# Kernel optimization log

Measured on AMD Instinct MI355X. Metric: run time of the kernel, lower is better.

Reference implementation:

```python
import jax, jax.numpy as jnp
import numpy as np

EPS = 1e-12
NUM_HEADS = 16
FEATURE_DIM = 16
HEAD_DIM = 64


def setup_inputs() -> dict:
    key = jax.random.key(0)
    k1, k2, k3, k4, k5 = jax.random.split(key, 5)
    b, l, d_model = 2, 2048, 1024
    scale = 0.02
    return {
        "hidden_states": jax.random.normal(k1, (b, l, d_model), jnp.float32),
        "Wq": jax.random.normal(k2, (FEATURE_DIM * NUM_HEADS, d_model), jnp.float32) * scale,
        "Wk": jax.random.normal(k3, (FEATURE_DIM * NUM_HEADS, d_model), jnp.float32) * scale,
        "Wv": jax.random.normal(k4, (NUM_HEADS * HEAD_DIM, d_model), jnp.float32) * scale,
        "Wo": jax.random.normal(k5, (d_model, NUM_HEADS * HEAD_DIM), jnp.float32) * scale,
    }


def reference(hidden_states, Wq, Wk, Wv, Wo):
    b, l, d_model = hidden_states.shape
    h, fd, hd = NUM_HEADS, FEATURE_DIM, HEAD_DIM
    # projections (no bias), split heads: (b, h, l, dim)
    q = (hidden_states @ Wq.T).reshape(b, l, h, fd).transpose(0, 2, 1, 3)
    k = (hidden_states @ Wk.T).reshape(b, l, h, fd).transpose(0, 2, 1, 3)
    v = (hidden_states @ Wv.T).reshape(b, l, h, hd).transpose(0, 2, 1, 3)
    # feature map is identity (default FeatureMap)
    # quadratic causal linear attention
    A_qk = jnp.einsum("bhnd,bhmd->bhnm", q, k)  # [b,h,l,l]
    A_qk = jnp.tril(A_qk)
    y = jnp.einsum("bhnm,bhme->bhne", A_qk, v)  # [b,h,l,hd]
    # denominator: q . cumsum(k)
    z = 1.0 / (jnp.einsum("bhld,bhld->bhl", q, jnp.cumsum(k, axis=2)) + EPS)
    y = y * z[..., None]
    # merge heads and output projection
    y = y.transpose(0, 2, 1, 3).reshape(b, l, h * hd)
    return y @ Wo.T
```

## Files before the change

kernel.cpp:

```cpp
#include <hip/hip_runtime.h>
#include <hip/hip_bf16.h>

#define NH 16
#define FD 16
#define HD 64
#define BATCH 2
#define SEQ 2048
#define DM 1024
#define ROWS (BATCH * SEQ)
#define CHUNK 128
#define NCH (SEQ / CHUNK)
#define NBH (BATCH * NH)

typedef __hip_bfloat16 bf16;
typedef __attribute__((ext_vector_type(8))) short short8;
typedef __attribute__((ext_vector_type(4))) float f32x4;

__device__ inline float bfbits(unsigned int h) {
  union { unsigned int u; float f; } c; c.u = h << 16; return c.f;
}
__device__ inline unsigned short f2bf(float x) {
  bf16 h = __float2bfloat16(x);
  return *(unsigned short*)&h;
}

__device__ inline void load8(const void* src, size_t idx, int isf32, float* out) {
  if (isf32) {
    const float* p = (const float*)src + idx;
    float4 a = *(const float4*)p;
    float4 b = *(const float4*)(p + 4);
    out[0] = a.x; out[1] = a.y; out[2] = a.z; out[3] = a.w;
    out[4] = b.x; out[5] = b.y; out[6] = b.z; out[7] = b.w;
  } else {
    const uint4 w = *(const uint4*)((const unsigned short*)src + idx);
    out[0] = bfbits(w.x & 0xffffu); out[1] = bfbits(w.x >> 16);
    out[2] = bfbits(w.y & 0xffffu); out[3] = bfbits(w.y >> 16);
    out[4] = bfbits(w.z & 0xffffu); out[5] = bfbits(w.z >> 16);
    out[6] = bfbits(w.w & 0xffffu); out[7] = bfbits(w.w >> 16);
  }
}

__device__ inline void gload16(const void* g, void* l) {
  __builtin_amdgcn_global_load_lds(
      (const __attribute__((address_space(1))) unsigned int*)g,
      (__attribute__((address_space(3))) unsigned int*)l, 16, 0, 0);
}

__global__ __launch_bounds__(256) void detect_dtype(const unsigned int* __restrict__ w,
                                                    int* __restrict__ flag) {
  __shared__ int red[256];
  int cnt = 0;
  for (int i = threadIdx.x; i < 4096; i += 256) {
    unsigned int e = (w[i] >> 7) & 0xFFu;
    cnt += (e >= 0x90u) ? 1 : 0;
  }
  red[threadIdx.x] = cnt;
  __syncthreads();
  for (int s = 128; s > 0; s >>= 1) {
    if (threadIdx.x < s) red[threadIdx.x] += red[threadIdx.x + s];
    __syncthreads();
  }
  if (threadIdx.x == 0) *flag = (red[0] > 64) ? 1 : 0;
}

__global__ __launch_bounds__(256, 2) void gemm_qk5(const void* __restrict__ A,
                                                   const void* __restrict__ Wq,
                                                   const void* __restrict__ Wk,
                                                   const int* __restrict__ flagp,
                                                   float* __restrict__ qf,
                                                   float* __restrict__ kf) {
  const int isf32 = *flagp;
  __shared__ float smem[9216];
  const int tid = threadIdx.x;
  const int h = tid >> 7;
  const int ltid = tid & 127;
  float* As = smem + h * 2304;
  float* Bs = smem + 4608 + h * 2304;
  const int m0 = blockIdx.x * 64;
  const int isK = blockIdx.y >> 2;
  const int n0 = (blockIdx.y & 3) * 64;
  const void* B = isK ? Wk : Wq;
  float* C = isK ? kf : qf;
  const int tx = ltid & 7;
  const int ty = ltid >> 3;
  const int lm = ltid >> 1, lcH = (ltid & 1) * 16;
  const int kbase = h * 512;
  double dacc[8][4];
#pragma unroll
  for (int i = 0; i < 8; ++i)
#pragma unroll
    for (int n = 0; n < 4; ++n) dacc[i][n] = 0.0;

  float av[16], bv[16];
  load8(A, (size_t)(m0 + lm) * DM + kbase + lcH, isf32, &av[0]);
  load8(A, (size_t)(m0 + lm) * DM + kbase + lcH + 8, isf32, &av[8]);
  load8(B, (size_t)(n0 + lm) * DM + kbase + lcH, isf32, &bv[0]);
  load8(B, (size_t)(n0 + lm) * DM + kbase + lcH + 8, isf32, &bv[8]);

  for (int t = 0; t < 16; ++t) {
    __syncthreads();
    *(float4*)&As[lm * 36 + lcH] = *(float4*)&av[0];
    *(float4*)&As[lm * 36 + lcH + 4] = *(float4*)&av[4];
    *(float4*)&As[lm * 36 + lcH + 8] = *(float4*)&av[8];
    *(float4*)&As[lm * 36 + lcH + 12] = *(float4*)&av[12];
    *(float4*)&Bs[lm * 36 + lcH] = *(float4*)&bv[0];
    *(float4*)&Bs[lm * 36 + lcH + 4] = *(float4*)&bv[4];
    *(float4*)&Bs[lm * 36 + lcH + 8] = *(float4*)&bv[8];
    *(float4*)&Bs[lm * 36 + lcH + 12] = *(float4*)&bv[12];
    __syncthreads();
    if (t < 15) {
      int kt = kbase + (t + 1) * 32;
      load8(A, (size_t)(m0 + lm) * DM + kt + lcH, isf32, &av[0]);
      load8(A, (size_t)(m0 + lm) * DM + kt + lcH + 8, isf32, &av[8]);
      load8(B, (size_t)(n0 + lm) * DM + kt + lcH, isf32, &bv[0]);
      load8(B, (size_t)(n0 + lm) * DM + kt + lcH + 8, isf32, &bv[8]);
    }
    for (int kk = 0; kk < 32; kk += 4) {
      float4 ar[8], br[4];
#pragma unroll
      for (int i = 0; i < 8; ++i) ar[i] = *(const float4*)&As[(tx + 8 * i) * 36 + kk];
#pragma unroll
      for (int n = 0; n < 4; ++n) br[n] = *(const float4*)&Bs[(ty * 4 + n) * 36 + kk];
      float facc[8][4] = {};
#pragma unroll
      for (int j = 0; j < 4; ++j) {
#pragma unroll
        for (int i = 0; i < 8; ++i) {
          float a = ((const float*)&ar[i])[j];
#pragma unroll
          for (int n = 0; n < 4; ++n)
            facc[i][n] += a * ((const float*)&br[n])[j];
        }
      }
#pragma unroll
      for (int i = 0; i < 8; ++i)
#pragma unroll
        for (int n = 0; n < 4; ++n) dacc[i][n] += (double)facc[i][n];
    }
  }

  double* dbl = (double*)smem;
  __syncthreads();
  if (h == 1) {
#pragma unroll
    for (int i = 0; i < 8; ++i)
#pragma unroll
      for (int n = 0; n < 4; ++n) dbl[ltid * 32 + i * 4 + n] = dacc[i][n];
  }
  __syncthreads();
  if (h == 0) {
#pragma unroll
    for (int i = 0; i < 8; ++i) {
#pragma unroll
      for (int n = 0; n < 4; ++n) dacc[i][n] += dbl[ltid * 32 + i * 4 + n];
      int row = m0 + tx + 8 * i;
      float4 o;
      o.x = (float)dacc[i][0]; o.y = (float)dacc[i][1];
      o.z = (float)dacc[i][2]; o.w = (float)dacc[i][3];
      *(float4*)&C[(size_t)row * 256 + n0 + ty * 4] = o;
    }
  }
}

template <int MODE>
__global__ __launch_bounds__(256) void gemm_mfma(const void* __restrict__ Ap,
                                                 const void* __restrict__ Bp,
                                                 const int* __restrict__ flagp,
                                                 void* __restrict__ Cp) {
  const int isf32 = *flagp;
  const int aF32 = (MODE == 0) ? isf32 : 0;
  const int bF32 = isf32;
  __shared__ unsigned short As[128 * 32];
  __shared__ unsigned short Bs[64 * 32];
  const int tid = threadIdx.x;
  const int wave = tid >> 6, lane = tid & 63;
  const int m0 = blockIdx.x * 128, n0 = blockIdx.y * 64;
  const int lrow = lane >> 2, lch = (lane & 3) * 8;
  const int wm = wave >> 1, wn = wave & 1;
  const int mlane = lane & 15, kgrp = lane >> 4;
  const unsigned short* Ab = (const unsigned short*)Ap;
  const unsigned short* Bb = (const unsigned short*)Bp;
  f32x4 acc[4][2];
#pragma unroll
  for (int t = 0; t < 4; ++t)
#pragma unroll
    for (int u = 0; u < 2; ++u) acc[t][u] = (f32x4){0.f, 0.f, 0.f, 0.f};

  for (int k0 = 0; k0 < DM; k0 += 32) {
    __syncthreads();
    if (!aF32) {
      const int r0 = wave * 32;
#pragma unroll
      for (int j = 0; j < 2; ++j) {
        const void* g = Ab + (size_t)(m0 + r0 + j * 16 + lrow) * DM + k0 + lch;
        gload16(g, &As[(r0 + j * 16) * 32]);
      }
    } else {
      for (int c = tid; c < 512; c += 256) {
        int r = c >> 2, cc = (c & 3) * 8;
        float v8[8];
        load8(Ap, (size_t)(m0 + r) * DM + k0 + cc, 1, v8);
        unsigned int w[4];
#pragma unroll
        for (int g2 = 0; g2 < 4; ++g2)
          w[g2] = (unsigned)f2bf(v8[2 * g2]) | ((unsigned)f2bf(v8[2 * g2 + 1]) << 16);
        *(uint4*)&As[r * 32 + cc] = *(uint4*)w;
      }
    }
    if (!bF32) {
      const void* g = Bb + (size_t)(n0 + wave * 16 + lrow) * DM + k0 + lch;
      gload16(g, &Bs[(wave * 16) * 32]);
    } else {
      {
        int c = tid;
        int r = c >> 2, cc = (c & 3) * 8;
        float v8[8];
        load8(Bp, (size_t)(n0 + r) * DM + k0 + cc, 1, v8);
        unsigned int w[4];
#pragma unroll
        for (int g2 = 0; g2 < 4; ++g2)
          w[g2] = (unsigned)f2bf(v8[2 * g2]) | ((unsigned)f2bf(v8[2 * g2 + 1]) << 16);
        *(uint4*)&Bs[r * 32 + cc] = *(uint4*)w;
      }
    }
    __syncthreads();

    short8 af[4], bfr[2];
#pragma unroll
    for (int t = 0; t < 4; ++t)
      af[t] = *(const short8*)&As[(wm * 64 + t * 16 + mlane) * 32 + kgrp * 8];
#pragma unroll
    for (int u = 0; u < 2; ++u)
      bfr[u] = *(const short8*)&Bs[(wn * 32 + u * 16 + mlane) * 32 + kgrp * 8];
#pragma unroll
    for (int t = 0; t < 4; ++t)
#pragma unroll
      for (int u = 0; u < 2; ++u)
        acc[t][u] = __builtin_amdgcn_mfma_f32_16x16x32_bf16(af[t], bfr[u], acc[t][u], 0, 0, 0);
  }

#pragma unroll
  for (int t = 0; t < 4; ++t)
#pragma unroll
    for (int u = 0; u < 2; ++u)
#pragma unroll
      for (int r = 0; r < 4; ++r) {
        int row = m0 + wm * 64 + t * 16 + kgrp * 4 + r;
        int col = n0 + wn * 32 + u * 16 + mlane;
        float v = acc[t][u][r];
        if (MODE == 0) {
          ((unsigned short*)Cp)[(size_t)row * DM + col] = f2bf(v);
        } else if (isf32) {
          ((float*)Cp)[(size_t)row * DM + col] = v;
        } else {
          ((unsigned short*)Cp)[(size_t)row * DM + col] = f2bf(v);
        }
      }
}

__global__ __launch_bounds__(256) void attn_intra(const float* __restrict__ qf,
                                                  const float* __restrict__ kf,
                                                  const unsigned short* __restrict__ vfb,
                                                  unsigned short* __restrict__ yib,
                                                  float* __restrict__ Sc,
                                                  double* __restrict__ Kc) {
  __shared__ float qc[CHUNK][20];
  __shared__ float kc[CHUNK][20];
  __shared__ float vc[CHUNK][68];
  const int bh = blockIdx.x >> 4;
  const int c = blockIdx.x & 15;
  const int b = bh >> 4, h = bh & 15;
  const int bl = c * CHUNK;
  const int tid = threadIdx.x;

  for (int idx = tid; idx < CHUNK * FD / 4; idx += 256) {
    int r = idx >> 2, f4 = (idx & 3) * 4;
    size_t g = ((size_t)(b * SEQ + bl + r)) * (NH * FD) + h * FD + f4;
    *(float4*)&qc[r][f4] = *(const float4*)&qf[g];
    *(float4*)&kc[r][f4] = *(const float4*)&kf[g];
  }
  for (int idx = tid; idx < CHUNK * HD / 8; idx += 256) {
    int r = idx >> 3, e8 = (idx & 7) * 8;
    uint4 w = *(const uint4*)&vfb[((size_t)(b * SEQ + bl + r)) * (NH * HD) + h * HD + e8];
    vc[r][e8 + 0] = bfbits(w.x & 0xffffu); vc[r][e8 + 1] = bfbits(w.x >> 16);
    vc[r][e8 + 2] = bfbits(w.y & 0xffffu); vc[r][e8 + 3] = bfbits(w.y >> 16);
    vc[r][e8 + 4] = bfbits(w.z & 0xffffu); vc[r][e8 + 5] = bfbits(w.z >> 16);
    vc[r][e8 + 6] = bfbits(w.w & 0xffffu); vc[r][e8 + 7] = bfbits(w.w >> 16);
  }
  __syncthreads();

  const int p = tid >> 2;
  const int n0 = 2 * p, n1 = 2 * p + 1;
  const int e0 = (tid & 3) * 16;
  float q0r[16], q1r[16];
#pragma unroll
  for (int d = 0; d < 16; ++d) { q0r[d] = qc[n0][d]; q1r[d] = qc[n1][d]; }
  float y0[16], y1[16];
#pragma unroll
  for (int e = 0; e < 16; ++e) { y0[e] = 0.f; y1[e] = 0.f; }

  for (int m = 0; m <= n1; ++m) {
    float kd[16], vv[16];
#pragma unroll
    for (int d = 0; d < 16; ++d) kd[d] = kc[m][d];
#pragma unroll
    for (int e = 0; e < 16; ++e) vv[e] = vc[m][e0 + e];
    float d0 = 0.f, d1 = 0.f;
#pragma unroll
    for (int d = 0; d < 16; ++d) { d0 += q0r[d] * kd[d]; d1 += q1r[d] * kd[d]; }
    if (m > n0) d0 = 0.f;
#pragma unroll
    for (int e = 0; e < 16; ++e) { y0[e] += d0 * vv[e]; y1[e] += d1 * vv[e]; }
  }
  const size_t ybase = (size_t)bh * SEQ + bl;
  {
    unsigned int w[4];
#pragma unroll
    for (int g = 0; g < 4; ++g)
      w[g] = (unsigned)f2bf(y0[2 * g]) | ((unsigned)f2bf(y0[2 * g + 1]) << 16);
    *(uint4*)&yib[(ybase + n0) * HD + e0] = *(uint4*)w;
#pragma unroll
    for (int g = 0; g < 4; ++g)
      w[g] = (unsigned)f2bf(y0[8 + 2 * g]) | ((unsigned)f2bf(y0[9 + 2 * g]) << 16);
    *(uint4*)&yib[(ybase + n0) * HD + e0 + 8] = *(uint4*)w;
#pragma unroll
    for (int g = 0; g < 4; ++g)
      w[g] = (unsigned)f2bf(y1[2 * g]) | ((unsigned)f2bf(y1[2 * g + 1]) << 16);
    *(uint4*)&yib[(ybase + n1) * HD + e0] = *(uint4*)w;
#pragma unroll
    for (int g = 0; g < 4; ++g)
      w[g] = (unsigned)f2bf(y1[8 + 2 * g]) | ((unsigned)f2bf(y1[9 + 2 * g]) << 16);
    *(uint4*)&yib[(ybase + n1) * HD + e0 + 8] = *(uint4*)w;
  }

  float* Scp = Sc + ((size_t)bh * NCH + c) * (FD * HD);
  for (int idx = tid; idx < FD * HD; idx += 256) {
    int d = idx >> 6, e = idx & 63;
    float s = 0.f;
    for (int m = 0; m < CHUNK; ++m) s += kc[m][d] * vc[m][e];
    Scp[idx] = s;
  }
  if (tid < FD) {
    double ks = 0.0;
    for (int m = 0; m < CHUNK; ++m) ks += (double)kc[m][tid];
    Kc[((size_t)bh * NCH + c) * FD + tid] = ks;
  }
}

__global__ __launch_bounds__(256) void scan_states(float* __restrict__ Sc,
                                                   double* __restrict__ Kc) {
  const int bh = blockIdx.x;
  const int tid = threadIdx.x;
  float4 acc = make_float4(0.f, 0.f, 0.f, 0.f);
  size_t base = (size_t)bh * NCH * (FD * HD) + (size_t)tid * 4;
  for (int c = 0; c < NCH; ++c) {
    float4* p = (float4*)(Sc + base + (size_t)c * (FD * HD));
    float4 v = *p;
    *p = acc;
    acc.x += v.x; acc.y += v.y; acc.z += v.z; acc.w += v.w;
  }
  if (tid < FD) {
    double a = 0.0;
    for (int c = 0; c < NCH; ++c) {
      size_t i = ((size_t)bh * NCH + c) * FD + tid;
      double t = Kc[i];
      Kc[i] = a;
      a += t;
    }
  }
}

__global__ __launch_bounds__(256) void attn_finish(const float* __restrict__ qf,
                                                   const float* __restrict__ kf,
                                                   const unsigned short* __restrict__ yib,
                                                   const float* __restrict__ Sc,
                                                   const double* __restrict__ Kc,
                                                   unsigned short* __restrict__ yob) {
  __shared__ float qc[CHUNK][20];
  __shared__ float kc[CHUNK][20];
  __shared__ float Sp[FD][HD];
  __shared__ double cs[CHUNK][17];
  __shared__ double zl[CHUNK];
  __shared__ double ksp[FD];
  const int bh = blockIdx.x >> 4;
  const int c = blockIdx.x & 15;
  const int b = bh >> 4, h = bh & 15;
  const int bl = c * CHUNK;
  const int tid = threadIdx.x;

  for (int idx = tid; idx < CHUNK * FD / 4; idx += 256) {
    int r = idx >> 2, f4 = (idx & 3) * 4;
    size_t g = ((size_t)(b * SEQ + bl + r)) * (NH * FD) + h * FD + f4;
    *(float4*)&qc[r][f4] = *(const float4*)&qf[g];
    *(float4*)&kc[r][f4] = *(const float4*)&kf[g];
  }
  const float* Scp = Sc + ((size_t)bh * NCH + c) * (FD * HD);
  for (int idx = tid; idx < FD * HD / 4; idx += 256) {
    int d = idx >> 4, e4 = (idx & 15) * 4;
    *(float4*)&Sp[d][e4] = *(const float4*)&Scp[(size_t)d * HD + e4];
  }
  if (tid < FD) ksp[tid] = Kc[((size_t)bh * NCH + c) * FD + tid];
  __syncthreads();

  if (tid < FD) {
    double run = ksp[tid];
    for (int m = 0; m < CHUNK; ++m) {
      run += (double)kc[m][tid];
      cs[m][tid] = run;
    }
  }
  __syncthreads();
  if (tid < CHUNK) {
    double dn = 0.0;
#pragma unroll
    for (int d = 0; d < 16; ++d) dn += (double)qc[tid][d] * cs[tid][d];
    zl[tid] = 1.0 / (dn + 1e-12);
  }
  __syncthreads();

  for (int idx = tid; idx < CHUNK * HD / 8; idx += 256) {
    int n = idx >> 3, e8 = (idx & 7) * 8;
    uint4 w = *(const uint4*)&yib[((size_t)bh * SEQ + bl + n) * HD + e8];
    float yv[8] = {bfbits(w.x & 0xffffu), bfbits(w.x >> 16),
                   bfbits(w.y & 0xffffu), bfbits(w.y >> 16),
                   bfbits(w.z & 0xffffu), bfbits(w.z >> 16),
                   bfbits(w.w & 0xffffu), bfbits(w.w >> 16)};
    double z = zl[n];
    unsigned int o[4];
#pragma unroll
    for (int jp = 0; jp < 4; ++jp) {
      int e = e8 + 2 * jp;
      float i0 = 0.f, i1 = 0.f;
#pragma unroll
      for (int d = 0; d < 16; ++d) {
        i0 += qc[n][d] * Sp[d][e];
        i1 += qc[n][d] * Sp[d][e + 1];
      }
      float r0 = (float)(((double)(yv[2 * jp] + i0)) * z);
      float r1 = (float)(((double)(yv[2 * jp + 1] + i1)) * z);
      o[jp] = (unsigned)f2bf(r0) | ((unsigned)f2bf(r1) << 16);
    }
    *(uint4*)&yob[((size_t)(b * SEQ + bl + n)) * (NH * HD) + h * HD + e8] = *(uint4*)o;
  }
}

extern "C" void kernel_launch(void* const* d_in, const int* in_sizes, int n_in,
                              void* d_out, int out_size, void* d_ws, size_t ws_size,
                              hipStream_t stream) {
  (void)in_sizes; (void)n_in; (void)out_size; (void)ws_size;
  const void* hs = d_in[0];
  const void* Wq = d_in[1];
  const void* Wk = d_in[2];
  const void* Wv = d_in[3];
  const void* Wo = d_in[4];

  char* ws = (char*)d_ws;
  float* qf = (float*)(ws);
  float* kf = (float*)(ws + (4u << 20));
  unsigned short* vfb = (unsigned short*)(ws + (8u << 20));
  unsigned short* yob = vfb;
  unsigned short* yib = (unsigned short*)(ws + (16u << 20));
  float* Sc = (float*)(ws + (24u << 20));
  double* Kc = (double*)(ws + (26u << 20));
  int* flag = (int*)(ws + (26u << 20) + 65536);

  detect_dtype<<<1, 256, 0, stream>>>((const unsigned int*)hs, flag);
  gemm_qk5<<<dim3(ROWS / 64, 8), 256, 0, stream>>>(hs, Wq, Wk, flag, qf, kf);
  gemm_mfma<0><<<dim3(ROWS / 128, 1024 / 64), 256, 0, stream>>>(hs, Wv, flag, vfb);
  attn_intra<<<NBH * NCH, 256, 0, stream>>>(qf, kf, vfb, yib, Sc, Kc);
  scan_states<<<NBH, 256, 0, stream>>>(Sc, Kc);
  attn_finish<<<NBH * NCH, 256, 0, stream>>>(qf, kf, yib, Sc, Kc, yob);
  gemm_mfma<1><<<dim3(ROWS / 128, 1024 / 64), 256, 0, stream>>>(yob, Wo, flag, d_out);
}
```

Baseline: 298.6 us.

## Merge Q/K and V projections into one interleaved launch, read B from global

Combines the fp64-accumulated Q/K projection kernel and the MFMA V projection kernel into a single launch whose even blocks do Q/K tiles and odd blocks do V tiles. This removes one launch and lets the two workloads share the GPU concurrently. The Q/K path no longer stages weights in shared memory; each thread loads its B slices directly from global memory. That shrinks LDS use so more blocks can be resident (launch bound raised to 4), but it adds redundant global/cache traffic. The double reduction buffer is also transposed to avoid bank conflicts, and the output GEMM is specialized to bf16 activations.

```diff
diff --git a/kernel.cpp b/kernel.cpp
--- a/kernel.cpp
+++ b/kernel.cpp
@@ -40,6 +40,15 @@
   }
 }
 
+__device__ inline float4 load4(const void* src, size_t idx, int isf32) {
+  if (isf32) return *((const float4*)((const float*)src + idx));
+  uint2 w = *(const uint2*)((const unsigned short*)src + idx);
+  float4 r;
+  r.x = bfbits(w.x & 0xffffu); r.y = bfbits(w.x >> 16);
+  r.z = bfbits(w.y & 0xffffu); r.w = bfbits(w.y >> 16);
+  return r;
+}
+
 __device__ inline void gload16(const void* g, void* l) {
   __builtin_amdgcn_global_load_lds(
       (const __attribute__((address_space(1))) unsigned int*)g,
@@ -63,113 +72,188 @@
   if (threadIdx.x == 0) *flag = (red[0] > 64) ? 1 : 0;
 }
 
-__global__ __launch_bounds__(256, 2) void gemm_qk5(const void* __restrict__ A,
-                                                   const void* __restrict__ Wq,
-                                                   const void* __restrict__ Wk,
-                                                   const int* __restrict__ flagp,
-                                                   float* __restrict__ qf,
-                                                   float* __restrict__ kf) {
+__global__ __launch_bounds__(256, 4) void stage1(const void* __restrict__ hs,
+                                                 const void* __restrict__ Wq,
+                                                 const void* __restrict__ Wk,
+                                                 const void* __restrict__ Wv,
+                                                 const int* __restrict__ flagp,
+                                                 float* __restrict__ qf,
+                                                 float* __restrict__ kf,
+                                                 unsigned short* __restrict__ vfb) {
+  __shared__ double2 smem_d2[2048];
   const int isf32 = *flagp;
-  __shared__ float smem[9216];
   const int tid = threadIdx.x;
-  const int h = tid >> 7;
-  const int ltid = tid & 127;
-  float* As = smem + h * 2304;
-  float* Bs = smem + 4608 + h * 2304;
-  const int m0 = blockIdx.x * 64;
-  const int isK = blockIdx.y >> 2;
-  const int n0 = (blockIdx.y & 3) * 64;
-  const void* B = isK ? Wk : Wq;
-  float* C = isK ? kf : qf;
-  const int tx = ltid & 7;
-  const int ty = ltid >> 3;
-  const int lm = ltid >> 1, lcH = (ltid & 1) * 16;
-  const int kbase = h * 512;
-  double dacc[8][4];
-#pragma unroll
-  for (int i = 0; i < 8; ++i)
-#pragma unroll
-    for (int n = 0; n < 4; ++n) dacc[i][n] = 0.0;
-
-  float av[16], bv[16];
-  load8(A, (size_t)(m0 + lm) * DM + kbase + lcH, isf32, &av[0]);
-  load8(A, (size_t)(m0 + lm) * DM + kbase + lcH + 8, isf32, &av[8]);
-  load8(B, (size_t)(n0 + lm) * DM + kbase + lcH, isf32, &bv[0]);
-  load8(B, (size_t)(n0 + lm) * DM + kbase + lcH + 8, isf32, &bv[8]);
-
-  for (int t = 0; t < 16; ++t) {
+
+  if ((blockIdx.x & 1) == 0) {
+    const int qid = blockIdx.x >> 1;
+    const int m0 = (qid & 63) * 64;
+    const int y = qid >> 6;
+    const int isK = y >> 2;
+    const int n0 = (y & 3) * 64;
+    const void* A = hs;
+    const void* B = isK ? Wk : Wq;
+    float* C = isK ? kf : qf;
+    const int h = tid >> 7;
+    const int ltid = tid & 127;
+    float* As = (float*)smem_d2 + h * 2304;
+    const int tx = ltid & 7;
+    const int ty = ltid >> 3;
+    const int lm = ltid >> 1, lcH = (ltid & 1) * 16;
+    const int kbase = h * 512;
+    double dacc[8][4];
+#pragma unroll
+    for (int i = 0; i < 8; ++i)
+#pragma unroll
+      for (int n = 0; n < 4; ++n) dacc[i][n] = 0.0;
+
+    float av[16];
+    load8(A, (size_t)(m0 + lm) * DM + kbase + lcH, isf32, &av[0]);
+    load8(A, (size_t)(m0 + lm) * DM + kbase + lcH + 8, isf32, &av[8]);
+
+    for (int t = 0; t < 16; ++t) {
+      __syncthreads();
+      *(float4*)&As[lm * 36 + lcH] = *(float4*)&av[0];
+      *(float4*)&As[lm * 36 + lcH + 4] = *(float4*)&av[4];
+      *(float4*)&As[lm * 36 + lcH + 8] = *(float4*)&av[8];
+      *(float4*)&As[lm * 36 + lcH + 12] = *(float4*)&av[12];
+      __syncthreads();
+      if (t < 15) {
+        int kt = kbase + (t + 1) * 32;
+        load8(A, (size_t)(m0 + lm) * DM + kt + lcH, isf32, &av[0]);
+        load8(A, (size_t)(m0 + lm) * DM + kt + lcH + 8, isf32, &av[8]);
+      }
+      const size_t bkt = kbase + t * 32;
+      for (int kk = 0; kk < 32; kk += 4) {
+        float4 ar[8], br[4];
+#pragma unroll
+        for (int i = 0; i < 8; ++i) ar[i] = *(const float4*)&As[(tx + 8 * i) * 36 + kk];
+#pragma unroll
+        for (int n = 0; n < 4; ++n)
+          br[n] = load4(B, (size_t)(n0 + ty * 4 + n) * DM + bkt + kk, isf32);
+        float facc[8][4] = {};
+#pragma unroll
+        for (int j = 0; j < 4; ++j) {
+#pragma unroll
+          for (int i = 0; i < 8; ++i) {
+            float a = ((const float*)&ar[i])[j];
+#pragma unroll
+            for (int n = 0; n < 4; ++n)
+              facc[i][n] += a * ((const float*)&br[n])[j];
+          }
+        }
+#pragma unroll
+        for (int i = 0; i < 8; ++i)
+#pragma unroll
+          for (int n = 0; n < 4; ++n) dacc[i][n] += (double)facc[i][n];
+      }
+    }
+
+    double* dbl = (double*)smem_d2;
     __syncthreads();
-    *(float4*)&As[lm * 36 + lcH] = *(float4*)&av[0];
-    *(float4*)&As[lm * 36 + lcH + 4] = *(float4*)&av[4];
-    *(float4*)&As[lm * 36 + lcH + 8] = *(float4*)&av[8];
-    *(float4*)&As[lm * 36 + lcH + 12] = *(float4*)&av[12];
-    *(float4*)&Bs[lm * 36 + lcH] = *(float4*)&bv[0];
-    *(float4*)&Bs[lm * 36 + lcH + 4] = *(float4*)&bv[4];
-    *(float4*)&Bs[lm * 36 + lcH + 8] = *(float4*)&bv[8];
-    *(float4*)&Bs[lm * 36 + lcH + 12] = *(float4*)&bv[12];
+    if (h == 1) {
+#pragma unroll
+      for (int i = 0; i < 8; ++i)
+#pragma unroll
+        for (int n = 0; n < 4; ++n) dbl[(i * 4 + n) * 128 + ltid] = dacc[i][n];
+    }
     __syncthreads();
-    if (t < 15) {
-      int kt = kbase + (t + 1) * 32;
-      load8(A, (size_t)(m0 + lm) * DM + kt + lcH, isf32, &av[0]);
-      load8(A, (size_t)(m0 + lm) * DM + kt + lcH + 8, isf32, &av[8]);
-      load8(B, (size_t)(n0 + lm) * DM + kt + lcH, isf32, &bv[0]);
-      load8(B, (size_t)(n0 + lm) * DM + kt + lcH + 8, isf32, &bv[8]);
-    }
-    for (int kk = 0; kk < 32; kk += 4) {
-      float4 ar[8], br[4];
-#pragma unroll
-      for (int i = 0; i < 8; ++i) ar[i] = *(const float4*)&As[(tx + 8 * i) * 36 + kk];
-#pragma unroll
-      for (int n = 0; n < 4; ++n) br[n] = *(const float4*)&Bs[(ty * 4 + n) * 36 + kk];
-      float facc[8][4] = {};
-#pragma unroll
-      for (int j = 0; j < 4; ++j) {
-#pragma unroll
-        for (int i = 0; i < 8; ++i) {
-          float a = ((const float*)&ar[i])[j];
-#pragma unroll
-          for (int n = 0; n < 4; ++n)
-            facc[i][n] += a * ((const float*)&br[n])[j];
+    if (h == 0) {
+#pragma unroll
+      for (int i = 0; i < 8; ++i) {
+#pragma unroll
+        for (int n = 0; n < 4; ++n) dacc[i][n] += dbl[(i * 4 + n) * 128 + ltid];
+        int row = m0 + tx + 8 * i;
+        float4 o;
+        o.x = (float)dacc[i][0]; o.y = (float)dacc[i][1];
+        o.z = (float)dacc[i][2]; o.w = (float)dacc[i][3];
+        *(float4*)&C[(size_t)row * 256 + n0 + ty * 4] = o;
+      }
+    }
+  } else {
+    const int vid = blockIdx.x >> 1;
+    const int m0 = (vid & 31) * 128;
+    const int n0 = (vid >> 5) * 64;
+    unsigned short* As = (unsigned short*)smem_d2;
+    unsigned short* Bs = As + 128 * 32;
+    const int wave = tid >> 6, lane = tid & 63;
+    const int lrow = lane >> 2, lch = (lane & 3) * 8;
+    const int wm = wave >> 1, wn = wave & 1;
+    const int mlane = lane & 15, kgrp = lane >> 4;
+    const unsigned short* Ab = (const unsigned short*)hs;
+    const unsigned short* Bb = (const unsigned short*)Wv;
+    f32x4 acc[4][2];
+#pragma unroll
+    for (int t = 0; t < 4; ++t)
+#pragma unroll
+      for (int u = 0; u < 2; ++u) acc[t][u] = (f32x4){0.f, 0.f, 0.f, 0.f};
+
+    for (int k0 = 0; k0 < DM; k0 += 32) {
+      __syncthreads();
+      if (!isf32) {
+        const int r0 = wave * 32;
+#pragma unroll
+        for (int j = 0; j < 2; ++j) {
+          const void* g = Ab + (size_t)(m0 + r0 + j * 16 + lrow) * DM + k0 + lch;
+          gload16(g, &As[(r0 + j * 16) * 32]);
         }
-      }
-#pragma unroll
-      for (int i = 0; i < 8; ++i)
-#pragma unroll
-        for (int n = 0; n < 4; ++n) dacc[i][n] += (double)facc[i][n];
-    }
-  }
-
-  double* dbl = (double*)smem;
-  __syncthreads();
-  if (h == 1) {
-#pragma unroll
-    for (int i = 0; i < 8; ++i)
-#pragma unroll
-      for (int n = 0; n < 4; ++n) dbl[ltid * 32 + i * 4 + n] = dacc[i][n];
-  }
-  __syncthreads();
-  if (h == 0) {
-#pragma unroll
-    for (int i = 0; i < 8; ++i) {
-#pragma unroll
-      for (int n = 0; n < 4; ++n) dacc[i][n] += dbl[ltid * 32 + i * 4 + n];
-      int row = m0 + tx + 8 * i;
-      float4 o;
-      o.x = (float)dacc[i][0]; o.y = (float)dacc[i][1];
-      o.z = (float)dacc[i][2]; o.w = (float)dacc[i][3];
-      *(float4*)&C[(size_t)row * 256 + n0 + ty * 4] = o;
-    }
-  }
-}
-
-template <int MODE>
-__global__ __launch_bounds__(256) void gemm_mfma(const void* __restrict__ Ap,
-                                                 const void* __restrict__ Bp,
-                                                 const int* __restrict__ flagp,
-                                                 void* __restrict__ Cp) {
+        const void* g = Bb + (size_t)(n0 + wave * 16 + lrow) * DM + k0 + lch;
+        gload16(g, &Bs[(wave * 16) * 32]);
+      } else {
+        for (int c = tid; c < 512; c += 256) {
+          int r = c >> 2, cc = (c & 3) * 8;
+          float v8[8];
+          load8(hs, (size_t)(m0 + r) * DM + k0 + cc, 1, v8);
+          unsigned int w[4];
+#pragma unroll
+          for (int g2 = 0; g2 < 4; ++g2)
+            w[g2] = (unsigned)f2bf(v8[2 * g2]) | ((unsigned)f2bf(v8[2 * g2 + 1]) << 16);
+          *(uint4*)&As[r * 32 + cc] = *(uint4*)w;
+        }
+        {
+          int r = tid >> 2, cc = (tid & 3) * 8;
+          float v8[8];
+          load8(Wv, (size_t)(n0 + r) * DM + k0 + cc, 1, v8);
+          unsigned int w[4];
+#pragma unroll
+          for (int g2 = 0; g2 < 4; ++g2)
+            w[g2] = (unsigned)f2bf(v8[2 * g2]) | ((unsigned)f2bf(v8[2 * g2 + 1]) << 16);
+          *(uint4*)&Bs[r * 32 + cc] = *(uint4*)w;
+        }
+      }
+      __syncthreads();
+
+      short8 af[4], bfr[2];
+#pragma unroll
+      for (int t = 0; t < 4; ++t)
+        af[t] = *(const short8*)&As[(wm * 64 + t * 16 + mlane) * 32 + kgrp * 8];
+#pragma unroll
+      for (int u = 0; u < 2; ++u)
+        bfr[u] = *(const short8*)&Bs[(wn * 32 + u * 16 + mlane) * 32 + kgrp * 8];
+#pragma unroll
+      for (int t = 0; t < 4; ++t)
+#pragma unroll
+        for (int u = 0; u < 2; ++u)
+          acc[t][u] = __builtin_amdgcn_mfma_f32_16x16x32_bf16(af[t], bfr[u], acc[t][u], 0, 0, 0);
+    }
+
+#pragma unroll
+    for (int t = 0; t < 4; ++t)
+#pragma unroll
+      for (int u = 0; u < 2; ++u)
+#pragma unroll
+        for (int r = 0; r < 4; ++r) {
+          int row = m0 + wm * 64 + t * 16 + kgrp * 4 + r;
+          int col = n0 + wn * 32 + u * 16 + mlane;
+          vfb[(size_t)row * DM + col] = f2bf(acc[t][u][r]);
+        }
+  }
+}
+
+__global__ __launch_bounds__(256) void gemm_o(const unsigned short* __restrict__ Ap,
+                                              const void* __restrict__ Bp,
+                                              const int* __restrict__ flagp,
+                                              void* __restrict__ Cp) {
   const int isf32 = *flagp;
-  const int aF32 = (MODE == 0) ? isf32 : 0;
-  const int bF32 = isf32;
   __shared__ unsigned short As[128 * 32];
   __shared__ unsigned short Bs[64 * 32];
   const int tid = threadIdx.x;
@@ -178,7 +262,6 @@
   const int lrow = lane >> 2, lch = (lane & 3) * 8;
   const int wm = wave >> 1, wn = wave & 1;
   const int mlane = lane & 15, kgrp = lane >> 4;
-  const unsigned short* Ab = (const unsigned short*)Ap;
   const unsigned short* Bb = (const unsigned short*)Bp;
   f32x4 acc[4][2];
 #pragma unroll
@@ -188,40 +271,26 @@
 
   for (int k0 = 0; k0 < DM; k0 += 32) {
     __syncthreads();
-    if (!aF32) {
+    {
       const int r0 = wave * 32;
 #pragma unroll
       for (int j = 0; j < 2; ++j) {
-        const void* g = Ab + (size_t)(m0 + r0 + j * 16 + lrow) * DM + k0 + lch;
+        const void* g = Ap + (size_t)(m0 + r0 + j * 16 + lrow) * DM + k0 + lch;
         gload16(g, &As[(r0 + j * 16) * 32]);
       }
-    } else {
-      for (int c = tid; c < 512; c += 256) {
-        int r = c >> 2, cc = (c & 3) * 8;
-        float v8[8];
-        load8(Ap, (size_t)(m0 + r) * DM + k0 + cc, 1, v8);
-        unsigned int w[4];
-#pragma unroll
-        for (int g2 = 0; g2 < 4; ++g2)
-          w[g2] = (unsigned)f2bf(v8[2 * g2]) | ((unsigned)f2bf(v8[2 * g2 + 1]) << 16);
-        *(uint4*)&As[r * 32 + cc] = *(uint4*)w;
-      }
-    }
-    if (!bF32) {
+    }
+    if (!isf32) {
       const void* g = Bb + (size_t)(n0 + wave * 16 + lrow) * DM + k0 + lch;
       gload16(g, &Bs[(wave * 16) * 32]);
     } else {
-      {
-        int c = tid;
-        int r = c >> 2, cc = (c & 3) * 8;
-        float v8[8];
-        load8(Bp, (size_t)(n0 + r) * DM + k0 + cc, 1, v8);
-        unsigned int w[4];
-#pragma unroll
-        for (int g2 = 0; g2 < 4; ++g2)
-          w[g2] = (unsigned)f2bf(v8[2 * g2]) | ((unsigned)f2bf(v8[2 * g2 + 1]) << 16);
-        *(uint4*)&Bs[r * 32 + cc] = *(uint4*)w;
-      }
+      int r = tid >> 2, cc = (tid & 3) * 8;
+      float v8[8];
+      load8(Bp, (size_t)(n0 + r) * DM + k0 + cc, 1, v8);
+      unsigned int w[4];
+#pragma unroll
+      for (int g2 = 0; g2 < 4; ++g2)
+        w[g2] = (unsigned)f2bf(v8[2 * g2]) | ((unsigned)f2bf(v8[2 * g2 + 1]) << 16);
+      *(uint4*)&Bs[r * 32 + cc] = *(uint4*)w;
     }
     __syncthreads();
 
@@ -248,13 +317,8 @@
         int row = m0 + wm * 64 + t * 16 + kgrp * 4 + r;
         int col = n0 + wn * 32 + u * 16 + mlane;
         float v = acc[t][u][r];
-        if (MODE == 0) {
-          ((unsigned short*)Cp)[(size_t)row * DM + col] = f2bf(v);
-        } else if (isf32) {
-          ((float*)Cp)[(size_t)row * DM + col] = v;
-        } else {
-          ((unsigned short*)Cp)[(size_t)row * DM + col] = f2bf(v);
-        }
+        if (isf32) ((float*)Cp)[(size_t)row * DM + col] = v;
+        else ((unsigned short*)Cp)[(size_t)row * DM + col] = f2bf(v);
       }
 }
 
@@ -465,10 +529,9 @@
   int* flag = (int*)(ws + (26u << 20) + 65536);
 
   detect_dtype<<<1, 256, 0, stream>>>((const unsigned int*)hs, flag);
-  gemm_qk5<<<dim3(ROWS / 64, 8), 256, 0, stream>>>(hs, Wq, Wk, flag, qf, kf);
-  gemm_mfma<0><<<dim3(ROWS / 128, 1024 / 64), 256, 0, stream>>>(hs, Wv, flag, vfb);
+  stage1<<<1024, 256, 0, stream>>>(hs, Wq, Wk, Wv, flag, qf, kf, vfb);
   attn_intra<<<NBH * NCH, 256, 0, stream>>>(qf, kf, vfb, yib, Sc, Kc);
   scan_states<<<NBH, 256, 0, stream>>>(Sc, Kc);
   attn_finish<<<NBH * NCH, 256, 0, stream>>>(qf, kf, yib, Sc, Kc, yob);
-  gemm_mfma<1><<<dim3(ROWS / 128, 1024 / 64), 256, 0, stream>>>(yob, Wo, flag, d_out);
-}
+  gemm_o<<<dim3(ROWS / 128, 1024 / 64), 256, 0, stream>>>(yob, Wo, flag, d_out);
+}
```

After: 862.0 us. +188.7%, slower.
